# Kernel optimization log

Measured on AMD Instinct MI355X. Metric: run time of the kernel, lower is better.

## Reference

```python
import jax, jax.numpy as jnp
import numpy as np

VOCAB = 40000
U = 128  # num_trans_units


def setup_inputs() -> dict:
    key = jax.random.key(0)
    ks = jax.random.split(key, 10)
    B, S, T, L = 16, 512, 64, 64
    sents = jax.random.randint(ks[0], (B, S), 0, 30000)
    triples = jax.random.randint(ks[1], (B, T, L, 3), 0, VOCAB)
    sent_triples = jax.random.randint(ks[2], (B, S, 1), 0, T)
    scale = 0.05
    emb_table = jax.random.normal(ks[3], (VOCAB, U), jnp.float32)
    W_trans = jax.random.normal(ks[4], (U, U), jnp.float32) * scale
    b_trans = jnp.zeros((U,), jnp.float32)
    W_ht = jax.random.normal(ks[5], (2 * U, U), jnp.float32) * scale
    b_ht = jnp.zeros((U,), jnp.float32)
    W_rel = jax.random.normal(ks[6], (U, U), jnp.float32) * scale
    b_rel = jnp.zeros((U,), jnp.float32)
    return {
        "sents": sents, "triples": triples, "sent_triples": sent_triples,
        "emb_table": emb_table,
        "W_trans": W_trans, "b_trans": b_trans,
        "W_ht": W_ht, "b_ht": b_ht,
        "W_rel": W_rel, "b_rel": b_rel,
    }


def reference(sents, triples, sent_triples, emb_table,
              W_trans, b_trans, W_ht, b_ht, W_rel, b_rel):
    # triples: [B, T, L, 3] int ids -> embed [B, T, L, 3, U]
    emb = emb_table[triples]
    # fc_trans_transform: Linear(U,U) + Tanh on last dim
    te = jnp.tanh(emb @ W_trans + b_trans)            # [B,T,L,3,U]
    head, relation, tail = te[..., 0, :], te[..., 1, :], te[..., 2, :]
    head_tail = jnp.concatenate([head, tail], axis=-1)  # [B,T,L,2U]
    ht_t = jnp.tanh(head_tail @ W_ht + b_ht)             # [B,T,L,U]
    rel_t = relation @ W_rel + b_rel                     # [B,T,L,U]
    e_weight = jnp.sum(rel_t * ht_t, axis=-1)            # [B,T,L]
    alpha = jax.nn.softmax(e_weight, axis=-1)            # over triple_len L
    graph_embed = jnp.sum(alpha[..., None] * head_tail, axis=2)  # [B,T,2U]
    # gather_nd: out[b, s] = graph_embed[b, sent_triples[b, s, 0]]
    idx = sent_triples[..., 0]                           # [B,S]
    out = jnp.take_along_axis(graph_embed, idx[:, :, None], axis=1)  # [B,S,2U]
    return out
```

## Files before the change

kernel.cpp:

```cpp
#include <hip/hip_runtime.h>
#include <cstdint>
#include <cstddef>

typedef short short8 __attribute__((ext_vector_type(8)));
typedef float f32x4 __attribute__((ext_vector_type(4)));

#define BB 16
#define SS 512
#define TT 64
#define LL 64
#define UU 128

#define WT_OFF    0u
#define WHT_OFF   (WT_OFF + 32768u)
#define WREL_OFF  (WHT_OFF + 65536u)

__device__ __forceinline__ unsigned short f2bf(float x) {
  unsigned u = __float_as_uint(x);
  unsigned r = ((u >> 16) & 1u) + 0x7FFFu;
  return (unsigned short)((u + r) >> 16);
}
__device__ __forceinline__ float ftanh(float x) {
  float e = __expf(2.0f * x);
  return 1.0f - __fdividef(2.0f, e + 1.0f);
}
__device__ __forceinline__ unsigned cvtpk(float a, float b) {
  unsigned r;
  asm("v_cvt_pk_bf16_f32 %0, %1, %2" : "=v"(r) : "v"(a), "v"(b));
  return r;
}
template<int CTRL>
__device__ __forceinline__ float dpp_mov(float x) {
  return __int_as_float(__builtin_amdgcn_update_dpp(
      0, __float_as_int(x), CTRL, 0xF, 0xF, true));
}
__device__ __forceinline__ float row16_sum(float x) {
  x += dpp_mov<0xB1>(x);
  x += dpp_mov<0x4E>(x);
  x += dpp_mov<0x141>(x);
  x += dpp_mov<0x140>(x);
  return x;
}
__device__ __forceinline__ float full64_sum(float x) {
  x = row16_sum(x);
  x += __shfl_xor(x, 16, 64);
  x += __shfl_xor(x, 32, 64);
  return x;
}
__device__ __forceinline__ float full64_max(float x) {
  x = fmaxf(x, dpp_mov<0xB1>(x));
  x = fmaxf(x, dpp_mov<0x4E>(x));
  x = fmaxf(x, dpp_mov<0x141>(x));
  x = fmaxf(x, dpp_mov<0x140>(x));
  x = fmaxf(x, __shfl_xor(x, 16, 64));
  x = fmaxf(x, __shfl_xor(x, 32, 64));
  return x;
}

__global__ void prep_kernel(const float* __restrict__ Wt,
                            const float* __restrict__ Wht,
                            const float* __restrict__ Wrel,
                            unsigned char* __restrict__ ws) {
  int slot = blockIdx.x * 256 + threadIdx.x;
  const float* W;
  unsigned char* base;
  if (slot < 2048)      { W = Wt;   base = ws + WT_OFF; }
  else if (slot < 6144) { W = Wht;  base = ws + WHT_OFF;  slot -= 2048; }
  else                  { W = Wrel; base = ws + WREL_OFF; slot -= 6144; }
  int lane = slot & 63, pair = slot >> 6;
  int n  = (pair & 7) * 16 + (lane & 15);
  int k0 = (pair >> 3) * 32 + (lane >> 4) * 8;
  short8 hv;
  #pragma unroll
  for (int j = 0; j < 8; ++j)
    hv[j] = (short)f2bf(W[(size_t)(k0 + j) * UU + n]);
  *reinterpret_cast<short8*>(base + (size_t)pair * 1024 + lane * 16) = hv;
}

__launch_bounds__(1024, 8)
__global__ void fused_bt(const int* __restrict__ triples,
                         const float* __restrict__ emb_f32,
                         const float* __restrict__ b_trans,
                         const float* __restrict__ b_ht,
                         const float* __restrict__ b_rel,
                         const int* __restrict__ sent_triples,
                         const unsigned char* __restrict__ wsr,
                         float* __restrict__ out) {
  __shared__ unsigned short TEB[192 * 128];
  __shared__ float EWt[8][64];
  __shared__ float PART[8][256];
  __shared__ int MATCH[512];
  __shared__ int NM;

  const int tid  = threadIdx.x;
  const int bt   = blockIdx.x;
  const int w    = tid >> 6;
  const int lane = tid & 63;
  const int li   = lane & 15;
  const int lg   = lane >> 4;
  const int nt   = w & 7;
  const int rh   = w >> 3;

  int tok[3];
  #pragma unroll
  for (int j = 0; j < 3; ++j) {
    int row = (tid + j * 1024) >> 4;
    tok[j] = triples[(size_t)bt * 192 + row];
  }
  int sidx = -1;
  if (tid < SS) sidx = sent_triples[(size_t)(bt >> 6) * SS + tid];
  if (tid == 0) NM = 0;

  float4 xv[3], yv[3];
  #pragma unroll
  for (int j = 0; j < 3; ++j) {
    int o = tid + j * 1024;
    int row = o >> 4, pc = o & 15;
    int clog = pc ^ (row & 15);
    const float* fb = emb_f32 + (size_t)tok[j] * UU + clog * 8;
    xv[j] = *reinterpret_cast<const float4*>(fb);
    yv[j] = *reinterpret_cast<const float4*>(fb + 4);
  }

  const unsigned char* wtb  = wsr + WT_OFF;
  const unsigned char* whtb = wsr + WHT_OFF;
  const unsigned char* wrlb = wsr + WREL_OFF;
  short8 B1h[4];
  #pragma unroll
  for (int kt = 0; kt < 4; ++kt)
    B1h[kt] = *reinterpret_cast<const short8*>(
        wtb + (size_t)(kt * 8 + nt) * 1024 + lane * 16);

  #pragma unroll
  for (int j = 0; j < 3; ++j) {
    int o = tid + j * 1024;
    uint4 pk = { cvtpk(xv[j].x, xv[j].y), cvtpk(xv[j].z, xv[j].w),
                 cvtpk(yv[j].x, yv[j].y), cvtpk(yv[j].z, yv[j].w) };
    *reinterpret_cast<uint4*>(&TEB[o * 8]) = pk;
  }

  const float bhv   = b_ht[nt * 16 + li];
  const float brlv  = b_rel[nt * 16 + li];
  const float4 btr4 = *reinterpret_cast<const float4*>(b_trans + nt * 16 + lg * 4);
  __syncthreads();

  if (sidx == (bt & 63))
    MATCH[atomicAdd(&NM, 1)] = tid;

  const int cc8 = nt * 2 + (lg >> 1);
  const int hb8 = (lg & 1) << 3;

  f32x4 acc[6];
  #pragma unroll
  for (int q = 0; q < 6; ++q) acc[q] = f32x4{0.f, 0.f, 0.f, 0.f};

  #pragma unroll
  for (int kt = 0; kt < 4; ++kt) {
    #pragma unroll
    for (int q = 0; q < 6; ++q) {
      const short8 b = *reinterpret_cast<const short8*>(
          &TEB[((rh * 6 + q) * 16 + li) * 128 + (((kt * 4 + lg) ^ li) << 3)]);
      acc[q] = __builtin_amdgcn_mfma_f32_16x16x32_bf16(B1h[kt], b, acc[q], 0, 0, 0);
    }
  }
  __syncthreads();

  #pragma unroll
  for (int q = 0; q < 6; ++q) {
    int row = (rh * 6 + q) * 16 + li;
    float v0 = ftanh(acc[q][0] + btr4.x);
    float v1 = ftanh(acc[q][1] + btr4.y);
    float v2 = ftanh(acc[q][2] + btr4.z);
    float v3 = ftanh(acc[q][3] + btr4.w);
    uint2 pk = { cvtpk(v0, v1), cvtpk(v2, v3) };
    *reinterpret_cast<uint2*>(
        reinterpret_cast<char*>(TEB) + row * 256 +
        (((cc8 ^ li) << 4) | hb8)) = pk;
  }

  short8 Wc = *reinterpret_cast<const short8*>(
      whtb + (size_t)nt * 1024 + lane * 16);
  __syncthreads();

  const int mh = rh * 2;
  f32x4 accH[2] = {{0.f,0.f,0.f,0.f},{0.f,0.f,0.f,0.f}};
  f32x4 accR[2] = {{0.f,0.f,0.f,0.f},{0.f,0.f,0.f,0.f}};

  #pragma unroll
  for (int kt = 0; kt < 8; ++kt) {
    short8 Wn;
    if (kt < 7)
      Wn = *reinterpret_cast<const short8*>(
          whtb + (size_t)((kt + 1) * 8 + nt) * 1024 + lane * 16);
    else
      Wn = *reinterpret_cast<const short8*>(
          wrlb + (size_t)nt * 1024 + lane * 16);
    const int koff = (kt < 4) ? 0 : 2;
    const int c16  = (kt & 3) * 4 + lg;
    #pragma unroll
    for (int mi = 0; mi < 2; ++mi) {
      const int row = 48 * (mh + mi) + 3 * li + koff;
      const short8 a = *reinterpret_cast<const short8*>(
          &TEB[row * 128 + ((c16 ^ (row & 15)) << 3)]);
      accH[mi] = __builtin_amdgcn_mfma_f32_16x16x32_bf16(a, Wc, accH[mi], 0, 0, 0);
    }
    Wc = Wn;
  }
  #pragma unroll
  for (int kt = 0; kt < 4; ++kt) {
    short8 Wn;
    if (kt < 3)
      Wn = *reinterpret_cast<const short8*>(
          wrlb + (size_t)((kt + 1) * 8 + nt) * 1024 + lane * 16);
    const int c16 = kt * 4 + lg;
    #pragma unroll
    for (int mi = 0; mi < 2; ++mi) {
      const int row = 48 * (mh + mi) + 3 * li + 1;
      const short8 a = *reinterpret_cast<const short8*>(
          &TEB[row * 128 + ((c16 ^ (row & 15)) << 3)]);
      accR[mi] = __builtin_amdgcn_mfma_f32_16x16x32_bf16(a, Wc, accR[mi], 0, 0, 0);
    }
    Wc = Wn;
  }

  #pragma unroll
  for (int mi = 0; mi < 2; ++mi) {
    #pragma unroll
    for (int r = 0; r < 4; ++r) {
      float p = ftanh(accH[mi][r] + bhv) * (accR[mi][r] + brlv);
      p = row16_sum(p);
      if (li == 0) EWt[nt][(mh + mi) * 16 + lg * 4 + r] = p;
    }
  }
  __syncthreads();

  float alpha;
  {
    float e = 0.f;
    #pragma unroll
    for (int n = 0; n < 8; ++n) e += EWt[n][lane];
    float mx = full64_max(e);
    float ex = __expf(e - mx);
    float sm = full64_sum(ex);
    alpha = ex / sm;
  }

  {
    int cp  = tid & 127, lgp = w >> 1;
    int c0  = cp << 1;
    int k   = (c0 >> 7) << 1;
    int cc  = c0 & 127;
    int w8  = cc >> 3, bofs = (cc & 7) << 1;
    float o0 = 0.f, o1 = 0.f;
    #pragma unroll
    for (int j = 0; j < 8; ++j) {
      int l = lgp * 8 + j;
      float al = __int_as_float(
          __builtin_amdgcn_readlane(__float_as_int(alpha), l));
      int row = 3 * l + k;
      unsigned u = *reinterpret_cast<const unsigned*>(
          reinterpret_cast<const char*>(TEB) + row * 256 +
          (((w8 ^ (row & 15)) << 4) | bofs));
      o0 = fmaf(al, __uint_as_float(u << 16), o0);
      o1 = fmaf(al, __uint_as_float(u & 0xFFFF0000u), o1);
    }
    *reinterpret_cast<float2*>(&PART[lgp][c0]) = make_float2(o0, o1);
  }
  __syncthreads();

  {
    const int b  = bt >> 6;
    const int nm = NM;
    if (w < nm) {
      float4 v = {0.f, 0.f, 0.f, 0.f};
      #pragma unroll
      for (int g = 0; g < 8; ++g) {
        float4 p = reinterpret_cast<const float4*>(&PART[g][0])[lane];
        v.x += p.x; v.y += p.y; v.z += p.z; v.w += p.w;
      }
      for (int q = w; q < nm; q += 16) {
        int s = MATCH[q];
        reinterpret_cast<float4*>(out + ((size_t)(b * SS + s)) * 256)[lane] = v;
      }
    }
  }
}

extern "C" void kernel_launch(void* const* d_in, const int* in_sizes, int n_in,
                              void* d_out, int out_size, void* d_ws, size_t ws_size,
                              hipStream_t stream) {
  const int*   triples      = (const int*)d_in[1];
  const int*   sent_triples = (const int*)d_in[2];
  const float* emb_table    = (const float*)d_in[3];
  const float* W_trans      = (const float*)d_in[4];
  const float* b_trans      = (const float*)d_in[5];
  const float* W_ht         = (const float*)d_in[6];
  const float* b_ht         = (const float*)d_in[7];
  const float* W_rel        = (const float*)d_in[8];
  const float* b_rel        = (const float*)d_in[9];
  float* out = (float*)d_out;
  unsigned char* ws = (unsigned char*)d_ws;

  prep_kernel<<<32, 256, 0, stream>>>(W_trans, W_ht, W_rel, ws);

  fused_bt<<<BB * TT, 1024, 0, stream>>>(
      triples, emb_table, b_trans, b_ht, b_rel, sent_triples, ws, out);
}
```

Baseline: 48.21 us.

## Precompute tanh(emb·W_trans+b) over the whole vocabulary, then gather bf16 rows

A new prep_te kernel applies the first linear layer and tanh to all 40000 vocabulary rows and writes them to workspace as bf16. The main kernel then gathers these transformed rows directly instead of gathering fp32 embeddings and running the first MFMA/tanh stage for every token. This removes redundant per-token transform work, since there are about five times more token slots than vocab rows, halves the gather bytes and drops one shared-memory phase and barrier. The cost is an extra launch plus a full pass over the embedding table and a 10MB intermediate write.

```diff
diff --git a/kernel.cpp b/kernel.cpp
--- a/kernel.cpp
+++ b/kernel.cpp
@@ -10,10 +10,12 @@
 #define TT 64
 #define LL 64
 #define UU 128
+#define NV 40000
 
 #define WT_OFF    0u
 #define WHT_OFF   (WT_OFF + 32768u)
 #define WREL_OFF  (WHT_OFF + 65536u)
+#define TE_OFF    (WREL_OFF + 32768u)
 
 __device__ __forceinline__ unsigned short f2bf(float x) {
   unsigned u = __float_as_uint(x);
@@ -78,9 +80,75 @@
 }
 
 __launch_bounds__(1024, 8)
+__global__ void prep_te(const float* __restrict__ emb_f32,
+                        const float* __restrict__ b_trans,
+                        const unsigned char* __restrict__ wsr,
+                        unsigned short* __restrict__ te_g) {
+  __shared__ unsigned short TEB[192 * 128];
+  const int tid  = threadIdx.x;
+  const int base = blockIdx.x * 192;
+  const int w    = tid >> 6;
+  const int lane = tid & 63;
+  const int li   = lane & 15;
+  const int lg   = lane >> 4;
+  const int nt   = w & 7;
+  const int rh   = w >> 3;
+
+  float4 xv[3], yv[3];
+  #pragma unroll
+  for (int j = 0; j < 3; ++j) {
+    int o = tid + j * 1024, row = o >> 4, pc = o & 15;
+    int grow = base + row; if (grow > NV - 1) grow = NV - 1;
+    int clog = pc ^ (row & 15);
+    const float* fb = emb_f32 + (size_t)grow * UU + clog * 8;
+    xv[j] = *reinterpret_cast<const float4*>(fb);
+    yv[j] = *reinterpret_cast<const float4*>(fb + 4);
+  }
+  const unsigned char* wtb = wsr + WT_OFF;
+  short8 B1h[4];
+  #pragma unroll
+  for (int kt = 0; kt < 4; ++kt)
+    B1h[kt] = *reinterpret_cast<const short8*>(
+        wtb + (size_t)(kt * 8 + nt) * 1024 + lane * 16);
+  #pragma unroll
+  for (int j = 0; j < 3; ++j) {
+    int o = tid + j * 1024;
+    uint4 pk = { cvtpk(xv[j].x, xv[j].y), cvtpk(xv[j].z, xv[j].w),
+                 cvtpk(yv[j].x, yv[j].y), cvtpk(yv[j].z, yv[j].w) };
+    *reinterpret_cast<uint4*>(&TEB[o * 8]) = pk;
+  }
+  const float4 btr4 = *reinterpret_cast<const float4*>(b_trans + nt * 16 + lg * 4);
+  __syncthreads();
+
+  f32x4 acc[6];
+  #pragma unroll
+  for (int q = 0; q < 6; ++q) acc[q] = f32x4{0.f, 0.f, 0.f, 0.f};
+  #pragma unroll
+  for (int kt = 0; kt < 4; ++kt) {
+    #pragma unroll
+    for (int q = 0; q < 6; ++q) {
+      const short8 b = *reinterpret_cast<const short8*>(
+          &TEB[((rh * 6 + q) * 16 + li) * 128 + (((kt * 4 + lg) ^ li) << 3)]);
+      acc[q] = __builtin_amdgcn_mfma_f32_16x16x32_bf16(B1h[kt], b, acc[q], 0, 0, 0);
+    }
+  }
+
+  #pragma unroll
+  for (int q = 0; q < 6; ++q) {
+    int row  = (rh * 6 + q) * 16 + li;
+    int grow = base + row; if (grow > NV - 1) grow = NV - 1;
+    float v0 = ftanh(acc[q][0] + btr4.x);
+    float v1 = ftanh(acc[q][1] + btr4.y);
+    float v2 = ftanh(acc[q][2] + btr4.z);
+    float v3 = ftanh(acc[q][3] + btr4.w);
+    uint2 pk = { cvtpk(v0, v1), cvtpk(v2, v3) };
+    *reinterpret_cast<uint2*>(te_g + (size_t)grow * UU + nt * 16 + lg * 4) = pk;
+  }
+}
+
+__launch_bounds__(1024, 8)
 __global__ void fused_bt(const int* __restrict__ triples,
-                         const float* __restrict__ emb_f32,
-                         const float* __restrict__ b_trans,
+                         const unsigned short* __restrict__ te_g,
                          const float* __restrict__ b_ht,
                          const float* __restrict__ b_rel,
                          const int* __restrict__ sent_triples,
@@ -111,76 +179,28 @@
   if (tid < SS) sidx = sent_triples[(size_t)(bt >> 6) * SS + tid];
   if (tid == 0) NM = 0;
 
-  float4 xv[3], yv[3];
+  short8 sv[3];
   #pragma unroll
   for (int j = 0; j < 3; ++j) {
-    int o = tid + j * 1024;
-    int row = o >> 4, pc = o & 15;
+    int o = tid + j * 1024, row = o >> 4, pc = o & 15;
     int clog = pc ^ (row & 15);
-    const float* fb = emb_f32 + (size_t)tok[j] * UU + clog * 8;
-    xv[j] = *reinterpret_cast<const float4*>(fb);
-    yv[j] = *reinterpret_cast<const float4*>(fb + 4);
-  }
-
-  const unsigned char* wtb  = wsr + WT_OFF;
+    sv[j] = *reinterpret_cast<const short8*>(
+        te_g + (size_t)tok[j] * UU + clog * 8);
+  }
+  #pragma unroll
+  for (int j = 0; j < 3; ++j)
+    *reinterpret_cast<short8*>(&TEB[(tid + j * 1024) * 8]) = sv[j];
+
   const unsigned char* whtb = wsr + WHT_OFF;
   const unsigned char* wrlb = wsr + WREL_OFF;
-  short8 B1h[4];
-  #pragma unroll
-  for (int kt = 0; kt < 4; ++kt)
-    B1h[kt] = *reinterpret_cast<const short8*>(
-        wtb + (size_t)(kt * 8 + nt) * 1024 + lane * 16);
-
-  #pragma unroll
-  for (int j = 0; j < 3; ++j) {
-    int o = tid + j * 1024;
-    uint4 pk = { cvtpk(xv[j].x, xv[j].y), cvtpk(xv[j].z, xv[j].w),
-                 cvtpk(yv[j].x, yv[j].y), cvtpk(yv[j].z, yv[j].w) };
-    *reinterpret_cast<uint4*>(&TEB[o * 8]) = pk;
-  }
-
-  const float bhv   = b_ht[nt * 16 + li];
-  const float brlv  = b_rel[nt * 16 + li];
-  const float4 btr4 = *reinterpret_cast<const float4*>(b_trans + nt * 16 + lg * 4);
-  __syncthreads();
-
-  if (sidx == (bt & 63))
-    MATCH[atomicAdd(&NM, 1)] = tid;
-
-  const int cc8 = nt * 2 + (lg >> 1);
-  const int hb8 = (lg & 1) << 3;
-
-  f32x4 acc[6];
-  #pragma unroll
-  for (int q = 0; q < 6; ++q) acc[q] = f32x4{0.f, 0.f, 0.f, 0.f};
-
-  #pragma unroll
-  for (int kt = 0; kt < 4; ++kt) {
-    #pragma unroll
-    for (int q = 0; q < 6; ++q) {
-      const short8 b = *reinterpret_cast<const short8*>(
-          &TEB[((rh * 6 + q) * 16 + li) * 128 + (((kt * 4 + lg) ^ li) << 3)]);
-      acc[q] = __builtin_amdgcn_mfma_f32_16x16x32_bf16(B1h[kt], b, acc[q], 0, 0, 0);
-    }
-  }
-  __syncthreads();
-
-  #pragma unroll
-  for (int q = 0; q < 6; ++q) {
-    int row = (rh * 6 + q) * 16 + li;
-    float v0 = ftanh(acc[q][0] + btr4.x);
-    float v1 = ftanh(acc[q][1] + btr4.y);
-    float v2 = ftanh(acc[q][2] + btr4.z);
-    float v3 = ftanh(acc[q][3] + btr4.w);
-    uint2 pk = { cvtpk(v0, v1), cvtpk(v2, v3) };
-    *reinterpret_cast<uint2*>(
-        reinterpret_cast<char*>(TEB) + row * 256 +
-        (((cc8 ^ li) << 4) | hb8)) = pk;
-  }
-
+  const float bhv  = b_ht[nt * 16 + li];
+  const float brlv = b_rel[nt * 16 + li];
   short8 Wc = *reinterpret_cast<const short8*>(
       whtb + (size_t)nt * 1024 + lane * 16);
   __syncthreads();
+
+  if (sidx == (bt & 63))
+    MATCH[atomicAdd(&NM, 1)] = tid;
 
   const int mh = rh * 2;
   f32x4 accH[2] = {{0.f,0.f,0.f,0.f},{0.f,0.f,0.f,0.f}};
@@ -300,9 +320,10 @@
   const float* b_rel        = (const float*)d_in[9];
   float* out = (float*)d_out;
   unsigned char* ws = (unsigned char*)d_ws;
+  unsigned short* te_g = (unsigned short*)(ws + TE_OFF);
 
   prep_kernel<<<32, 256, 0, stream>>>(W_trans, W_ht, W_rel, ws);
-
+  prep_te<<<(NV + 191) / 192, 1024, 0, stream>>>(emb_table, b_trans, ws, te_g);
   fused_bt<<<BB * TT, 1024, 0, stream>>>(
-      triples, emb_table, b_trans, b_ht, b_rel, sent_triples, ws, out);
-}
+      triples, te_g, b_ht, b_rel, sent_triples, ws, out);
+}
```

New measurement: 43.36 us. -10.1%, faster.

## Precompute per-vocabulary transformed embeddings and projections, then gather per triple

Applied to the files above, without the earlier changes.

A new prep_all kernel runs over the whole embedding table. For every vocab row it computes the tanh transform and three projections: the head half of W_ht with its bias, the tail half of W_ht, and W_rel with its bias. It stores them in workspace as bf16 and fp32. The main kernel then gathers these precomputed rows per triple, so it no longer runs MFMAs per triple; it only does tanh(A+B)·R, the softmax and the weighted sum. This cuts matrix work to the vocab size (40000 rows versus 196608 triple slots) but adds roughly 70MB of workspace writes plus larger random gathers of fp32 rows.

```diff
diff --git a/kernel.cpp b/kernel.cpp
--- a/kernel.cpp
+++ b/kernel.cpp
@@ -10,10 +10,15 @@
 #define TT 64
 #define LL 64
 #define UU 128
+#define NV 40000
 
 #define WT_OFF    0u
 #define WHT_OFF   (WT_OFF + 32768u)
 #define WREL_OFF  (WHT_OFF + 65536u)
+#define TE_OFF    (WREL_OFF + 32768u)
+#define A_OFF     (TE_OFF  + 40000u*128u*2u)
+#define B2_OFF    (A_OFF   + 40000u*128u*4u)
+#define R_OFF     (B2_OFF  + 40000u*128u*4u)
 
 __device__ __forceinline__ unsigned short f2bf(float x) {
   unsigned u = __float_as_uint(x);
@@ -77,23 +82,19 @@
   *reinterpret_cast<short8*>(base + (size_t)pair * 1024 + lane * 16) = hv;
 }
 
-__launch_bounds__(1024, 8)
-__global__ void fused_bt(const int* __restrict__ triples,
-                         const float* __restrict__ emb_f32,
+__launch_bounds__(1024, 4)
+__global__ void prep_all(const float* __restrict__ emb_f32,
                          const float* __restrict__ b_trans,
                          const float* __restrict__ b_ht,
                          const float* __restrict__ b_rel,
-                         const int* __restrict__ sent_triples,
                          const unsigned char* __restrict__ wsr,
-                         float* __restrict__ out) {
+                         unsigned short* __restrict__ te_g,
+                         float* __restrict__ A_g,
+                         float* __restrict__ B_g,
+                         float* __restrict__ R_g) {
   __shared__ unsigned short TEB[192 * 128];
-  __shared__ float EWt[8][64];
-  __shared__ float PART[8][256];
-  __shared__ int MATCH[512];
-  __shared__ int NM;
-
   const int tid  = threadIdx.x;
-  const int bt   = blockIdx.x;
+  const int base = blockIdx.x * 192;
   const int w    = tid >> 6;
   const int lane = tid & 63;
   const int li   = lane & 15;
@@ -101,27 +102,16 @@
   const int nt   = w & 7;
   const int rh   = w >> 3;
 
-  int tok[3];
+  float4 xv[3], yv[3];
   #pragma unroll
   for (int j = 0; j < 3; ++j) {
-    int row = (tid + j * 1024) >> 4;
-    tok[j] = triples[(size_t)bt * 192 + row];
-  }
-  int sidx = -1;
-  if (tid < SS) sidx = sent_triples[(size_t)(bt >> 6) * SS + tid];
-  if (tid == 0) NM = 0;
-
-  float4 xv[3], yv[3];
-  #pragma unroll
-  for (int j = 0; j < 3; ++j) {
-    int o = tid + j * 1024;
-    int row = o >> 4, pc = o & 15;
+    int o = tid + j * 1024, row = o >> 4, pc = o & 15;
+    int grow = base + row; if (grow > NV - 1) grow = NV - 1;
     int clog = pc ^ (row & 15);
-    const float* fb = emb_f32 + (size_t)tok[j] * UU + clog * 8;
+    const float* fb = emb_f32 + (size_t)grow * UU + clog * 8;
     xv[j] = *reinterpret_cast<const float4*>(fb);
     yv[j] = *reinterpret_cast<const float4*>(fb + 4);
   }
-
   const unsigned char* wtb  = wsr + WT_OFF;
   const unsigned char* whtb = wsr + WHT_OFF;
   const unsigned char* wrlb = wsr + WREL_OFF;
@@ -130,7 +120,6 @@
   for (int kt = 0; kt < 4; ++kt)
     B1h[kt] = *reinterpret_cast<const short8*>(
         wtb + (size_t)(kt * 8 + nt) * 1024 + lane * 16);
-
   #pragma unroll
   for (int j = 0; j < 3; ++j) {
     int o = tid + j * 1024;
@@ -138,22 +127,12 @@
                  cvtpk(yv[j].x, yv[j].y), cvtpk(yv[j].z, yv[j].w) };
     *reinterpret_cast<uint4*>(&TEB[o * 8]) = pk;
   }
-
-  const float bhv   = b_ht[nt * 16 + li];
-  const float brlv  = b_rel[nt * 16 + li];
   const float4 btr4 = *reinterpret_cast<const float4*>(b_trans + nt * 16 + lg * 4);
   __syncthreads();
 
-  if (sidx == (bt & 63))
-    MATCH[atomicAdd(&NM, 1)] = tid;
-
-  const int cc8 = nt * 2 + (lg >> 1);
-  const int hb8 = (lg & 1) << 3;
-
   f32x4 acc[6];
   #pragma unroll
   for (int q = 0; q < 6; ++q) acc[q] = f32x4{0.f, 0.f, 0.f, 0.f};
-
   #pragma unroll
   for (int kt = 0; kt < 4; ++kt) {
     #pragma unroll
@@ -165,80 +144,120 @@
   }
   __syncthreads();
 
+  const int cc8 = nt * 2 + (lg >> 1);
+  const int hb8 = (lg & 1) << 3;
   #pragma unroll
   for (int q = 0; q < 6; ++q) {
-    int row = (rh * 6 + q) * 16 + li;
+    int row  = (rh * 6 + q) * 16 + li;
+    int grow = base + row; if (grow > NV - 1) grow = NV - 1;
     float v0 = ftanh(acc[q][0] + btr4.x);
     float v1 = ftanh(acc[q][1] + btr4.y);
     float v2 = ftanh(acc[q][2] + btr4.z);
     float v3 = ftanh(acc[q][3] + btr4.w);
     uint2 pk = { cvtpk(v0, v1), cvtpk(v2, v3) };
     *reinterpret_cast<uint2*>(
-        reinterpret_cast<char*>(TEB) + row * 256 +
-        (((cc8 ^ li) << 4) | hb8)) = pk;
-  }
-
-  short8 Wc = *reinterpret_cast<const short8*>(
-      whtb + (size_t)nt * 1024 + lane * 16);
-  __syncthreads();
-
-  const int mh = rh * 2;
-  f32x4 accH[2] = {{0.f,0.f,0.f,0.f},{0.f,0.f,0.f,0.f}};
-  f32x4 accR[2] = {{0.f,0.f,0.f,0.f},{0.f,0.f,0.f,0.f}};
-
-  #pragma unroll
-  for (int kt = 0; kt < 8; ++kt) {
-    short8 Wn;
-    if (kt < 7)
-      Wn = *reinterpret_cast<const short8*>(
-          whtb + (size_t)((kt + 1) * 8 + nt) * 1024 + lane * 16);
-    else
-      Wn = *reinterpret_cast<const short8*>(
-          wrlb + (size_t)nt * 1024 + lane * 16);
-    const int koff = (kt < 4) ? 0 : 2;
-    const int c16  = (kt & 3) * 4 + lg;
-    #pragma unroll
-    for (int mi = 0; mi < 2; ++mi) {
-      const int row = 48 * (mh + mi) + 3 * li + koff;
-      const short8 a = *reinterpret_cast<const short8*>(
-          &TEB[row * 128 + ((c16 ^ (row & 15)) << 3)]);
-      accH[mi] = __builtin_amdgcn_mfma_f32_16x16x32_bf16(a, Wc, accH[mi], 0, 0, 0);
-    }
-    Wc = Wn;
-  }
-  #pragma unroll
-  for (int kt = 0; kt < 4; ++kt) {
-    short8 Wn;
-    if (kt < 3)
-      Wn = *reinterpret_cast<const short8*>(
-          wrlb + (size_t)((kt + 1) * 8 + nt) * 1024 + lane * 16);
-    const int c16 = kt * 4 + lg;
-    #pragma unroll
-    for (int mi = 0; mi < 2; ++mi) {
-      const int row = 48 * (mh + mi) + 3 * li + 1;
-      const short8 a = *reinterpret_cast<const short8*>(
-          &TEB[row * 128 + ((c16 ^ (row & 15)) << 3)]);
-      accR[mi] = __builtin_amdgcn_mfma_f32_16x16x32_bf16(a, Wc, accR[mi], 0, 0, 0);
-    }
-    Wc = Wn;
-  }
-
-  #pragma unroll
-  for (int mi = 0; mi < 2; ++mi) {
-    #pragma unroll
-    for (int r = 0; r < 4; ++r) {
-      float p = ftanh(accH[mi][r] + bhv) * (accR[mi][r] + brlv);
-      p = row16_sum(p);
-      if (li == 0) EWt[nt][(mh + mi) * 16 + lg * 4 + r] = p;
-    }
-  }
-  __syncthreads();
+        reinterpret_cast<char*>(TEB) + row * 256 + (((cc8 ^ li) << 4) | hb8)) = pk;
+    *reinterpret_cast<uint2*>(te_g + (size_t)grow * UU + nt * 16 + lg * 4) = pk;
+  }
+  __syncthreads();
+
+  const float4 bht4 = *reinterpret_cast<const float4*>(b_ht + nt * 16 + lg * 4);
+  const float4 brl4 = *reinterpret_cast<const float4*>(b_rel + nt * 16 + lg * 4);
+  #pragma unroll
+  for (int pass = 0; pass < 3; ++pass) {
+    const unsigned char* wb = (pass == 2) ? wrlb : whtb;
+    const int ktoff = (pass == 1) ? 4 : 0;
+    f32x4 a2[6];
+    #pragma unroll
+    for (int q = 0; q < 6; ++q) a2[q] = f32x4{0.f, 0.f, 0.f, 0.f};
+    #pragma unroll
+    for (int kt = 0; kt < 4; ++kt) {
+      const short8 Wf = *reinterpret_cast<const short8*>(
+          wb + (size_t)((kt + ktoff) * 8 + nt) * 1024 + lane * 16);
+      #pragma unroll
+      for (int q = 0; q < 6; ++q) {
+        const short8 b = *reinterpret_cast<const short8*>(
+            &TEB[((rh * 6 + q) * 16 + li) * 128 + (((kt * 4 + lg) ^ li) << 3)]);
+        a2[q] = __builtin_amdgcn_mfma_f32_16x16x32_bf16(Wf, b, a2[q], 0, 0, 0);
+      }
+    }
+    float* out_g = (pass == 0) ? A_g : (pass == 1) ? B_g : R_g;
+    float4 bias = (pass == 0) ? bht4
+               : (pass == 2) ? brl4 : float4{0.f, 0.f, 0.f, 0.f};
+    #pragma unroll
+    for (int q = 0; q < 6; ++q) {
+      int row  = (rh * 6 + q) * 16 + li;
+      int grow = base + row; if (grow > NV - 1) grow = NV - 1;
+      float4 v = { a2[q][0] + bias.x, a2[q][1] + bias.y,
+                   a2[q][2] + bias.z, a2[q][3] + bias.w };
+      *reinterpret_cast<float4*>(out_g + (size_t)grow * UU + nt * 16 + lg * 4) = v;
+    }
+  }
+}
+
+__launch_bounds__(1024, 8)
+__global__ void fused_bt(const int* __restrict__ triples,
+                         const unsigned short* __restrict__ te_g,
+                         const float* __restrict__ A_g,
+                         const float* __restrict__ B_g,
+                         const float* __restrict__ R_g,
+                         const int* __restrict__ sent_triples,
+                         float* __restrict__ out) {
+  __shared__ unsigned short TEB[128 * 128];
+  __shared__ float EWt[64];
+  __shared__ float PART[8][256];
+  __shared__ int MATCH[512];
+  __shared__ int NM;
+
+  const int tid  = threadIdx.x;
+  const int bt   = blockIdx.x;
+  const int w    = tid >> 6;
+  const int lane = tid & 63;
+  const int l    = tid >> 4;
+  const int d8   = tid & 15;
+
+  const int* tb = triples + (size_t)bt * 192;
+  const int th = tb[3 * l], tr = tb[3 * l + 1], tt = tb[3 * l + 2];
+
+  int sidx = -1;
+  if (tid < SS) sidx = sent_triples[(size_t)(bt >> 6) * SS + tid];
+  if (tid == 0) NM = 0;
+
+  short8 svh = *reinterpret_cast<const short8*>(te_g + (size_t)th * UU + d8 * 8);
+  short8 svt = *reinterpret_cast<const short8*>(te_g + (size_t)tt * UU + d8 * 8);
+
+  const float* Ap = A_g + (size_t)th * UU + d8 * 8;
+  const float* Bp = B_g + (size_t)tt * UU + d8 * 8;
+  const float* Rp = R_g + (size_t)tr * UU + d8 * 8;
+  float4 a0 = *reinterpret_cast<const float4*>(Ap);
+  float4 a1 = *reinterpret_cast<const float4*>(Ap + 4);
+  float4 b0 = *reinterpret_cast<const float4*>(Bp);
+  float4 b1 = *reinterpret_cast<const float4*>(Bp + 4);
+  float4 r0 = *reinterpret_cast<const float4*>(Rp);
+  float4 r1 = *reinterpret_cast<const float4*>(Rp + 4);
+
+  *reinterpret_cast<short8*>(&TEB[(l * 16 + d8) * 8]) = svh;
+  *reinterpret_cast<short8*>(&TEB[((64 + l) * 16 + d8) * 8]) = svt;
+
+  float p = 0.f;
+  p = fmaf(ftanh(a0.x + b0.x), r0.x, p);
+  p = fmaf(ftanh(a0.y + b0.y), r0.y, p);
+  p = fmaf(ftanh(a0.z + b0.z), r0.z, p);
+  p = fmaf(ftanh(a0.w + b0.w), r0.w, p);
+  p = fmaf(ftanh(a1.x + b1.x), r1.x, p);
+  p = fmaf(ftanh(a1.y + b1.y), r1.y, p);
+  p = fmaf(ftanh(a1.z + b1.z), r1.z, p);
+  p = fmaf(ftanh(a1.w + b1.w), r1.w, p);
+  p = row16_sum(p);
+  if (d8 == 0) EWt[l] = p;
+  __syncthreads();
+
+  if (sidx == (bt & 63))
+    MATCH[atomicAdd(&NM, 1)] = tid;
 
   float alpha;
   {
-    float e = 0.f;
-    #pragma unroll
-    for (int n = 0; n < 8; ++n) e += EWt[n][lane];
+    float e = EWt[lane];
     float mx = full64_max(e);
     float ex = __expf(e - mx);
     float sm = full64_sum(ex);
@@ -248,19 +267,17 @@
   {
     int cp  = tid & 127, lgp = w >> 1;
     int c0  = cp << 1;
-    int k   = (c0 >> 7) << 1;
+    int k   = c0 >> 7;
     int cc  = c0 & 127;
-    int w8  = cc >> 3, bofs = (cc & 7) << 1;
     float o0 = 0.f, o1 = 0.f;
     #pragma unroll
     for (int j = 0; j < 8; ++j) {
-      int l = lgp * 8 + j;
+      int lr  = lgp * 8 + j;
       float al = __int_as_float(
-          __builtin_amdgcn_readlane(__float_as_int(alpha), l));
-      int row = 3 * l + k;
+          __builtin_amdgcn_readlane(__float_as_int(alpha), lr));
+      int row = (k << 6) + lr;
       unsigned u = *reinterpret_cast<const unsigned*>(
-          reinterpret_cast<const char*>(TEB) + row * 256 +
-          (((w8 ^ (row & 15)) << 4) | bofs));
+          reinterpret_cast<const char*>(TEB) + row * 256 + cc * 2);
       o0 = fmaf(al, __uint_as_float(u << 16), o0);
       o1 = fmaf(al, __uint_as_float(u & 0xFFFF0000u), o1);
     }
@@ -275,8 +292,8 @@
       float4 v = {0.f, 0.f, 0.f, 0.f};
       #pragma unroll
       for (int g = 0; g < 8; ++g) {
-        float4 p = reinterpret_cast<const float4*>(&PART[g][0])[lane];
-        v.x += p.x; v.y += p.y; v.z += p.z; v.w += p.w;
+        float4 pp = reinterpret_cast<const float4*>(&PART[g][0])[lane];
+        v.x += pp.x; v.y += pp.y; v.z += pp.z; v.w += pp.w;
       }
       for (int q = w; q < nm; q += 16) {
         int s = MATCH[q];
@@ -300,9 +317,14 @@
   const float* b_rel        = (const float*)d_in[9];
   float* out = (float*)d_out;
   unsigned char* ws = (unsigned char*)d_ws;
+  unsigned short* te_g = (unsigned short*)(ws + TE_OFF);
+  float* A_g = (float*)(ws + A_OFF);
+  float* B_g = (float*)(ws + B2_OFF);
+  float* R_g = (float*)(ws + R_OFF);
 
   prep_kernel<<<32, 256, 0, stream>>>(W_trans, W_ht, W_rel, ws);
-
+  prep_all<<<(NV + 191) / 192, 1024, 0, stream>>>(
+      emb_table, b_trans, b_ht, b_rel, ws, te_g, A_g, B_g, R_g);
   fused_bt<<<BB * TT, 1024, 0, stream>>>(
-      triples, emb_table, b_trans, b_ht, b_rel, sent_triples, ws, out);
-}
+      triples, te_g, A_g, B_g, R_g, sent_triples, ws ? out : out);
+}
```

Measured after the change: 53.73 us. 11.5% more time.
